# Performance work log

Measured on AMD Instinct MI355X. Metric: run time of the kernel, lower is better.

## Reference

```python
import jax, jax.numpy as jnp
import numpy as np


def setup_inputs() -> dict:
    key = jax.random.key(0)
    kp, kq, kr = jax.random.split(key, 3)
    N, M = 8192, 4096
    points = jax.random.normal(kp, (N, 3), dtype=jnp.float32)
    queries = jax.random.normal(kq, (M, 3), dtype=jnp.float32)
    radii = jax.random.uniform(kr, (M,), dtype=jnp.float32) * 0.3 + 0.1
    points_row_splits = jnp.array([0, N], dtype=jnp.int64)
    queries_row_splits = jnp.array([0, M], dtype=jnp.int64)
    return {
        "points": points,
        "queries": queries,
        "radii": radii,
        "points_row_splits": points_row_splits,
        "queries_row_splits": queries_row_splits,
    }


def reference(points, queries, radii, points_row_splits, queries_row_splits):
    """Radius search, metric=L2 (squared distances), return_distances=True.

    JIT-friendly ragged encoding: neighbors_index and neighbors_distance are
    returned as fixed-size [M*N] buffers with valid entries packed at the
    front (query-major order, matching the compact list of the original op);
    padding is -1 for indices and 0.0 for distances. neighbors_row_splits is
    the exact exclusive prefix sum of per-query neighbor counts ([M+1]).
    """
    M = queries.shape[0]
    N = points.shape[0]
    # squared L2 distances [M, N] without materializing [M, N, 3]
    q2 = jnp.sum(queries * queries, axis=1, keepdims=True)          # [M,1]
    p2 = jnp.sum(points * points, axis=1)[None, :]                  # [1,N]
    qp = jnp.einsum("md,nd->mn", queries, points)                   # [M,N]
    d2 = jnp.maximum(q2 + p2 - 2.0 * qp, 0.0)

    mask = d2 <= (radii * radii)[:, None]                           # [M,N]
    counts = jnp.sum(mask, axis=1, dtype=jnp.int64)                 # [M]
    neighbors_row_splits = jnp.concatenate(
        [jnp.zeros((1,), jnp.int64), jnp.cumsum(counts)])           # [M+1]
    total = neighbors_row_splits[-1]

    # Stable sort of the flattened (row-major) mask packs all valid slots at
    # the front while preserving query-major, point-index order.
    flat_mask = mask.reshape(-1)
    order = jnp.argsort(1 - flat_mask.astype(jnp.int32), stable=True)  # [M*N]
    valid = jnp.arange(M * N, dtype=jnp.int64) < total
    neighbors_index = jnp.where(valid, (order % N).astype(jnp.int64), -1)
    neighbors_distance = jnp.where(valid, d2.reshape(-1)[order], 0.0)
    return neighbors_index, neighbors_row_splits, neighbors_distance
```

## Files before the change

kernel.cpp:

```cpp
#include <hip/hip_runtime.h>


typedef float f32x4 __attribute__((ext_vector_type(4)));

__global__ __launch_bounds__(256) void rs_fused(
    const float* __restrict__ pts, const float* __restrict__ qs,
    const float* __restrict__ rad, int* __restrict__ counts,
    unsigned long long* __restrict__ masks, int storeMasks,
    float* __restrict__ out_idx, float* __restrict__ out_dist,
    long long MN, int N, int M) {
    int t = threadIdx.x;
    int wv = t >> 6, lane = t & 63;
    int gw = blockIdx.x * 4 + wv;
    int nWaves = gridDim.x * 4;

    bool hasQ = (gw < M);
    int qc = hasQ ? gw : 0;
    float qx = qs[3 * qc], qy = qs[3 * qc + 1], qz = qs[3 * qc + 2];
    float q2 = __fadd_rn(__fadd_rn(__fmul_rn(qx, qx), __fmul_rn(qy, qy)),
                         __fmul_rn(qz, qz));
    float r = rad[qc];
    float r2 = hasQ ? __fmul_rn(r, r) : -1.0f;

    int nc = N >> 6;
    int vecIters = N >> 8;
    long long V = MN >> 2;
    long long perWave = (V + nWaves - 1) / nWaves;
    int fillIters = (int)((perWave + 63) >> 6);
    long long fbase = (long long)gw * perWave;
    long long fend = fbase + perWave;
    if (fend > V) fend = V;
    f32x4* vidx = (f32x4*)out_idx;
    f32x4* vdst = (f32x4*)out_dist;
    f32x4 vm1 = {-1.0f, -1.0f, -1.0f, -1.0f};
    f32x4 vz = {0.0f, 0.0f, 0.0f, 0.0f};

    int iters = vecIters > fillIters ? vecIters : fillIters;
    int cntLane = 0;
    int shift = (lane & 15) << 2;
    int wordSel = lane >> 4;

    for (int it = 0; it < iters; ++it) {
        if (it < fillIters) {
            long long fi = fbase + (long long)it * 64 + lane;
            if (fi < fend) { vidx[fi] = vm1; vdst[fi] = vz; }
        }
        if (it < vecIters) {
            const f32x4* pv = (const f32x4*)(pts + (size_t)it * 768);
            f32x4 v0 = pv[3 * lane + 0];
            f32x4 v1 = pv[3 * lane + 1];
            f32x4 v2 = pv[3 * lane + 2];
            float px[4] = {v0.x, v0.w, v1.z, v2.y};
            float py[4] = {v0.y, v1.x, v1.w, v2.z};
            float pz[4] = {v0.z, v1.y, v2.x, v2.w};
            unsigned nib = 0;
#pragma unroll
            for (int k = 0; k < 4; ++k) {
                float p2 = __fadd_rn(
                    __fadd_rn(__fmul_rn(px[k], px[k]), __fmul_rn(py[k], py[k])),
                    __fmul_rn(pz[k], pz[k]));
                float qp = __fadd_rn(
                    __fadd_rn(__fmul_rn(qx, px[k]), __fmul_rn(qy, py[k])),
                    __fmul_rn(qz, pz[k]));
                float d2 = __fsub_rn(__fadd_rn(q2, p2), __fmul_rn(2.0f, qp));
                bool pred = (d2 <= r2);
                nib |= (pred ? 1u : 0u) << k;
                cntLane += pred ? 1 : 0;
            }
            unsigned long long contrib = (unsigned long long)nib << shift;
#pragma unroll
            for (int s = 1; s < 16; s <<= 1) contrib |= __shfl_xor(contrib, s, 64);
            if (storeMasks && hasQ && (lane & 15) == 0)
                masks[(long long)gw * nc + (it << 2) + wordSel] = contrib;
        }
    }
    for (int c = vecIters << 2; c < nc; ++c) {
        int p = (c << 6) + lane;
        bool vld = (p < N);
        int pcl = vld ? p : 0;
        float px = pts[3 * pcl], py = pts[3 * pcl + 1], pz = pts[3 * pcl + 2];
        float p2 = __fadd_rn(__fadd_rn(__fmul_rn(px, px), __fmul_rn(py, py)),
                             __fmul_rn(pz, pz));
        float qp = __fadd_rn(__fadd_rn(__fmul_rn(qx, px), __fmul_rn(qy, py)),
                             __fmul_rn(qz, pz));
        float d2 = __fsub_rn(__fadd_rn(q2, p2), __fmul_rn(2.0f, qp));
        bool pred = vld && (d2 <= r2);
        unsigned long long b = __ballot(pred);
        if (storeMasks && hasQ && lane == 0) masks[(long long)gw * nc + c] = b;
        cntLane += pred ? 1 : 0;
    }
    for (int off = 32; off > 0; off >>= 1) cntLane += __shfl_down(cntLane, off, 64);
    if (hasQ && lane == 0) counts[gw] = cntLane;
}

__global__ __launch_bounds__(256) void rs_write(
    const float* __restrict__ pts, const float* __restrict__ qs,
    const float* __restrict__ rad,
    const int* __restrict__ counts, const unsigned long long* __restrict__ masks,
    int useMasks,
    float* __restrict__ out_idx, float* __restrict__ out_splits,
    float* __restrict__ out_dist, int N, int M) {
    __shared__ int s_scan[256];
    __shared__ int s_split[4097];
    int t = threadIdx.x;

    {
        int c[16];
        int sum = 0;
        int b16 = t * 16;
#pragma unroll
        for (int i = 0; i < 16; ++i) {
            int idx = b16 + i;
            int v = (idx < M) ? counts[idx] : 0;
            c[i] = sum;
            sum += v;
        }
        s_scan[t] = sum;
        __syncthreads();
        for (int off = 1; off < 256; off <<= 1) {
            int add = (t >= off) ? s_scan[t - off] : 0;
            __syncthreads();
            s_scan[t] += add;
            __syncthreads();
        }
        int excl = (t == 0) ? 0 : s_scan[t - 1];
#pragma unroll
        for (int i = 0; i < 16; ++i)
            if (b16 + i < M) s_split[b16 + i] = excl + c[i];
        if (t == 255) s_split[M] = excl + sum;
        __syncthreads();
    }

    if (blockIdx.x == 0) {
        for (int i = t; i <= M; i += 256) out_splits[i] = (float)s_split[i];
    }

    int wv = t >> 6, lane = t & 63;
    int w = blockIdx.x * 4 + wv;
    if (w >= M) return;
    float qxx = qs[3 * w], qyy = qs[3 * w + 1], qzz = qs[3 * w + 2];
    float q2 = __fadd_rn(__fadd_rn(__fmul_rn(qxx, qxx), __fmul_rn(qyy, qyy)),
                         __fmul_rn(qzz, qzz));
    long long base = s_split[w];
    int nc = N >> 6;

    if (useMasks) {
        const unsigned long long* mq = masks + (long long)w * nc;
        unsigned long long w0 = (lane < nc) ? mq[lane] : 0ull;
        unsigned long long w1 = (lane + 64 < nc) ? mq[lane + 64] : 0ull;
        int c0 = __popcll(w0), c1 = __popcll(w1);
        int i0 = c0, i1 = c1;
        for (int off = 1; off < 64; off <<= 1) {
            int t0 = __shfl_up(i0, off, 64);
            int t1 = __shfl_up(i1, off, 64);
            if (lane >= off) { i0 += t0; i1 += t1; }
        }
        int total0 = __shfl(i0, 63, 64);

        long long o = base + (i0 - c0);
        int pbase = lane << 6;
        unsigned long long mm = w0;
        while (mm) {
            int b = __ffsll((long long)mm) - 1;
            int p = pbase + b;
            float px = pts[3 * p], py = pts[3 * p + 1], pz = pts[3 * p + 2];
            float p2 = __fadd_rn(__fadd_rn(__fmul_rn(px, px), __fmul_rn(py, py)),
                                 __fmul_rn(pz, pz));
            float qp = __fadd_rn(__fadd_rn(__fmul_rn(qxx, px), __fmul_rn(qyy, py)),
                                 __fmul_rn(qzz, pz));
            float d2 = fmaxf(__fsub_rn(__fadd_rn(q2, p2), __fmul_rn(2.0f, qp)), 0.0f);
            out_idx[o] = (float)p;
            out_dist[o] = d2;
            ++o;
            mm &= mm - 1;
        }
        o = base + total0 + (i1 - c1);
        pbase = (lane + 64) << 6;
        mm = w1;
        while (mm) {
            int b = __ffsll((long long)mm) - 1;
            int p = pbase + b;
            float px = pts[3 * p], py = pts[3 * p + 1], pz = pts[3 * p + 2];
            float p2 = __fadd_rn(__fadd_rn(__fmul_rn(px, px), __fmul_rn(py, py)),
                                 __fmul_rn(pz, pz));
            float qp = __fadd_rn(__fadd_rn(__fmul_rn(qxx, px), __fmul_rn(qyy, py)),
                                 __fmul_rn(qzz, pz));
            float d2 = fmaxf(__fsub_rn(__fadd_rn(q2, p2), __fmul_rn(2.0f, qp)), 0.0f);
            out_idx[o] = (float)p;
            out_dist[o] = d2;
            ++o;
            mm &= mm - 1;
        }
    } else {
        float r = rad[w];
        float r2 = __fmul_rn(r, r);
        int cum = 0;
        unsigned long long lanemask = (1ull << lane) - 1ull;
        for (int p0 = 0; p0 < N; p0 += 64) {
            int p = p0 + lane;
            float px = pts[3 * p], py = pts[3 * p + 1], pz = pts[3 * p + 2];
            float p2 = __fadd_rn(__fadd_rn(__fmul_rn(px, px), __fmul_rn(py, py)),
                                 __fmul_rn(pz, pz));
            float qp = __fadd_rn(__fadd_rn(__fmul_rn(qxx, px), __fmul_rn(qyy, py)),
                                 __fmul_rn(qzz, pz));
            float d2 = __fsub_rn(__fadd_rn(q2, p2), __fmul_rn(2.0f, qp));
            bool pred = (d2 <= r2);
            unsigned long long mask = __ballot(pred);
            if (pred) {
                long long pos = base + cum + __popcll(mask & lanemask);
                out_idx[pos] = (float)p;
                out_dist[pos] = fmaxf(d2, 0.0f);
            }
            cum += __popcll(mask);
        }
    }
}

extern "C" void kernel_launch(void* const* d_in, const int* in_sizes, int n_in,
                              void* d_out, int out_size, void* d_ws, size_t ws_size,
                              hipStream_t stream) {
    const float* points = (const float*)d_in[0];
    const float* queries = (const float*)d_in[1];
    const float* radii = (const float*)d_in[2];
    int N = in_sizes[0] / 3;
    int M = in_sizes[1] / 3;
    long long MN = (long long)M * (long long)N;

    float* out = (float*)d_out;
    float* out_idx = out;
    float* out_splits = out + MN;
    float* out_dist = out + MN + M + 1;

    char* ws = (char*)d_ws;
    size_t off = 0;
    auto take = [&](size_t bytes) -> size_t {
        size_t o = off;
        off += (bytes + 255) & ~(size_t)255;
        return o;
    };
    size_t o_counts = take((size_t)M * 4);
    size_t o_masks = take((size_t)M * (size_t)(N / 64) * 8);
    bool useMasks = (off <= ws_size) && ((N >> 6) <= 128);
    int* counts = (int*)(ws + o_counts);
    unsigned long long* masks = (unsigned long long*)(ws + o_masks);

    int C = (M + 3) / 4;
    rs_fused<<<C, 256, 0, stream>>>(points, queries, radii, counts, masks,
                                    useMasks ? 1 : 0, out_idx, out_dist, MN, N, M);
    int writeBlocks = (M + 3) / 4;
    rs_write<<<writeBlocks, 256, 0, stream>>>(points, queries, radii, counts, masks,
                                              useMasks ? 1 : 0, out_idx, out_splits,
                                              out_dist, N, M);
}
```

Before: 58.91 us.

## Skip zero-filling the distance region that later gets overwritten

The first kernel used to zero-fill the whole distance buffer before the real distances were written. That fill now happens in the second kernel, where interleaved blocks compute the total count and zero only the padding tail past it. This removes a redundant write of the valid distance prefix. It also rebalances where memory traffic lands across the two kernels, and each fill block repeats a reduction over all counts.

```diff
diff --git a/kernel.cpp b/kernel.cpp
--- a/kernel.cpp
+++ b/kernel.cpp
@@ -2,13 +2,24 @@
 
 
 typedef float f32x4 __attribute__((ext_vector_type(4)));
+
+__device__ __forceinline__ void fill_region(float* __restrict__ base, long long n,
+                                            float val, long long tid, long long nth) {
+    long long head = (long long)(((16u - ((unsigned)(size_t)base & 15u)) & 15u) >> 2);
+    if (head > n) head = n;
+    for (long long i = tid; i < head; i += nth) base[i] = val;
+    long long nv = (n - head) >> 2;
+    f32x4* v = (f32x4*)(base + head);
+    f32x4 vv = {val, val, val, val};
+    for (long long i = tid; i < nv; i += nth) v[i] = vv;
+    for (long long i = head + (nv << 2) + tid; i < n; i += nth) base[i] = val;
+}
 
 __global__ __launch_bounds__(256) void rs_fused(
     const float* __restrict__ pts, const float* __restrict__ qs,
     const float* __restrict__ rad, int* __restrict__ counts,
     unsigned long long* __restrict__ masks, int storeMasks,
-    float* __restrict__ out_idx, float* __restrict__ out_dist,
-    long long MN, int N, int M) {
+    float* __restrict__ out_idx, long long MN, int N, int M) {
     int t = threadIdx.x;
     int wv = t >> 6, lane = t & 63;
     int gw = blockIdx.x * 4 + wv;
@@ -31,9 +42,7 @@
     long long fend = fbase + perWave;
     if (fend > V) fend = V;
     f32x4* vidx = (f32x4*)out_idx;
-    f32x4* vdst = (f32x4*)out_dist;
     f32x4 vm1 = {-1.0f, -1.0f, -1.0f, -1.0f};
-    f32x4 vz = {0.0f, 0.0f, 0.0f, 0.0f};
 
     int iters = vecIters > fillIters ? vecIters : fillIters;
     int cntLane = 0;
@@ -43,7 +52,7 @@
     for (int it = 0; it < iters; ++it) {
         if (it < fillIters) {
             long long fi = fbase + (long long)it * 64 + lane;
-            if (fi < fend) { vidx[fi] = vm1; vdst[fi] = vz; }
+            if (fi < fend) vidx[fi] = vm1;
         }
         if (it < vecIters) {
             const f32x4* pv = (const f32x4*)(pts + (size_t)it * 768);
@@ -99,10 +108,37 @@
     const int* __restrict__ counts, const unsigned long long* __restrict__ masks,
     int useMasks,
     float* __restrict__ out_idx, float* __restrict__ out_splits,
-    float* __restrict__ out_dist, int N, int M) {
+    float* __restrict__ out_dist, long long MN, int N, int M, int W ) {
     __shared__ int s_scan[256];
     __shared__ int s_split[4097];
     int t = threadIdx.x;
+    int bid = blockIdx.x;
+
+    if (bid & 1) {
+        int fid = bid >> 1;
+        int sum = 0;
+        int b16 = t * 16;
+#pragma unroll
+        for (int i = 0; i < 16; ++i) {
+            int idx = b16 + i;
+            if (idx < M) sum += counts[idx];
+        }
+        s_scan[t] = sum;
+        __syncthreads();
+        for (int off = 128; off > 0; off >>= 1) {
+            if (t < off) s_scan[t] += s_scan[t + off];
+            __syncthreads();
+        }
+        long long total = s_scan[0];
+        long long padLen = MN - total;
+        if (padLen > 0) {
+            long long tid = (long long)fid * 256 + t;
+            long long nth = (long long)W * 256;
+            fill_region(out_dist + total, padLen, 0.0f, tid, nth);
+        }
+        return;
+    }
+    int wb = bid >> 1;
 
     {
         int c[16];
@@ -131,12 +167,12 @@
         __syncthreads();
     }
 
-    if (blockIdx.x == 0) {
+    if (wb == 0) {
         for (int i = t; i <= M; i += 256) out_splits[i] = (float)s_split[i];
     }
 
     int wv = t >> 6, lane = t & 63;
-    int w = blockIdx.x * 4 + wv;
+    int w = wb * 4 + wv;
     if (w >= M) return;
     float qxx = qs[3 * w], qyy = qs[3 * w + 1], qzz = qs[3 * w + 2];
     float q2 = __fadd_rn(__fadd_rn(__fmul_rn(qxx, qxx), __fmul_rn(qyy, qyy)),
@@ -246,9 +282,9 @@
 
     int C = (M + 3) / 4;
     rs_fused<<<C, 256, 0, stream>>>(points, queries, radii, counts, masks,
-                                    useMasks ? 1 : 0, out_idx, out_dist, MN, N, M);
-    int writeBlocks = (M + 3) / 4;
-    rs_write<<<writeBlocks, 256, 0, stream>>>(points, queries, radii, counts, masks,
-                                              useMasks ? 1 : 0, out_idx, out_splits,
-                                              out_dist, N, M);
-}
+                                    useMasks ? 1 : 0, out_idx, MN, N, M);
+    int W = (M + 3) / 4;
+    rs_write<<<2 * W, 256, 0, stream>>>(points, queries, radii, counts, masks,
+                                        useMasks ? 1 : 0, out_idx, out_splits,
+                                        out_dist, MN, N, M, W);
+}
```

Measured after the change: 77.02 us. 1.31x slower.

## Move prefix scan into last-finishing block of count kernel

Applied to the files above, without the earlier changes.

Before, every block of the write kernel redid the full prefix scan over all query counts in shared memory. Now the last block to finish the count kernel, found with an atomic counter and threadfence, does the scan once and writes the splits to global memory. The pack kernel then just reads its base offset. This adds a memset launch and a serialized tail scan at the end of the first kernel, and also clamps out-of-range point loads in the non-mask path.

```diff
diff --git a/kernel.cpp b/kernel.cpp
--- a/kernel.cpp
+++ b/kernel.cpp
@@ -8,7 +8,8 @@
     const float* __restrict__ rad, int* __restrict__ counts,
     unsigned long long* __restrict__ masks, int storeMasks,
     float* __restrict__ out_idx, float* __restrict__ out_dist,
-    long long MN, int N, int M) {
+    float* __restrict__ out_splits, int* __restrict__ splits_i,
+    int* __restrict__ done, long long MN, int N, int M) {
     int t = threadIdx.x;
     int wv = t >> 6, lane = t & 63;
     int gw = blockIdx.x * 4 + wv;
@@ -91,27 +92,25 @@
     }
     for (int off = 32; off > 0; off >>= 1) cntLane += __shfl_down(cntLane, off, 64);
     if (hasQ && lane == 0) counts[gw] = cntLane;
-}
-
-__global__ __launch_bounds__(256) void rs_write(
-    const float* __restrict__ pts, const float* __restrict__ qs,
-    const float* __restrict__ rad,
-    const int* __restrict__ counts, const unsigned long long* __restrict__ masks,
-    int useMasks,
-    float* __restrict__ out_idx, float* __restrict__ out_splits,
-    float* __restrict__ out_dist, int N, int M) {
+
+    __shared__ int s_last;
     __shared__ int s_scan[256];
-    __shared__ int s_split[4097];
-    int t = threadIdx.x;
-
-    {
+    __syncthreads();
+    if (t == 0) {
+        __threadfence();
+        int old = atomicAdd(done, 1);
+        s_last = (old == (int)gridDim.x - 1) ? 1 : 0;
+    }
+    __syncthreads();
+    if (s_last) {
+        volatile const int* vcounts = (volatile const int*)counts;
         int c[16];
         int sum = 0;
         int b16 = t * 16;
 #pragma unroll
         for (int i = 0; i < 16; ++i) {
             int idx = b16 + i;
-            int v = (idx < M) ? counts[idx] : 0;
+            int v = (idx < M) ? vcounts[idx] : 0;
             c[i] = sum;
             sum += v;
         }
@@ -125,23 +124,35 @@
         }
         int excl = (t == 0) ? 0 : s_scan[t - 1];
 #pragma unroll
-        for (int i = 0; i < 16; ++i)
-            if (b16 + i < M) s_split[b16 + i] = excl + c[i];
-        if (t == 255) s_split[M] = excl + sum;
-        __syncthreads();
-    }
-
-    if (blockIdx.x == 0) {
-        for (int i = t; i <= M; i += 256) out_splits[i] = (float)s_split[i];
-    }
-
+        for (int i = 0; i < 16; ++i) {
+            int idx = b16 + i;
+            if (idx < M) {
+                int v = excl + c[i];
+                splits_i[idx] = v;
+                out_splits[idx] = (float)v;
+            }
+        }
+        if (t == 255) {
+            splits_i[M] = excl + sum;
+            out_splits[M] = (float)(excl + sum);
+        }
+    }
+}
+
+__global__ __launch_bounds__(256) void rs_pack(
+    const float* __restrict__ pts, const float* __restrict__ qs,
+    const float* __restrict__ rad,
+    const int* __restrict__ splits_i, const unsigned long long* __restrict__ masks,
+    int useMasks,
+    float* __restrict__ out_idx, float* __restrict__ out_dist, int N, int M) {
+    int t = threadIdx.x;
     int wv = t >> 6, lane = t & 63;
     int w = blockIdx.x * 4 + wv;
     if (w >= M) return;
     float qxx = qs[3 * w], qyy = qs[3 * w + 1], qzz = qs[3 * w + 2];
     float q2 = __fadd_rn(__fadd_rn(__fmul_rn(qxx, qxx), __fmul_rn(qyy, qyy)),
                          __fmul_rn(qzz, qzz));
-    long long base = s_split[w];
+    long long base = splits_i[w];
     int nc = N >> 6;
 
     if (useMasks) {
@@ -198,13 +209,15 @@
         unsigned long long lanemask = (1ull << lane) - 1ull;
         for (int p0 = 0; p0 < N; p0 += 64) {
             int p = p0 + lane;
-            float px = pts[3 * p], py = pts[3 * p + 1], pz = pts[3 * p + 2];
+            bool vld = (p < N);
+            int pcl = vld ? p : 0;
+            float px = pts[3 * pcl], py = pts[3 * pcl + 1], pz = pts[3 * pcl + 2];
             float p2 = __fadd_rn(__fadd_rn(__fmul_rn(px, px), __fmul_rn(py, py)),
                                  __fmul_rn(pz, pz));
             float qp = __fadd_rn(__fadd_rn(__fmul_rn(qxx, px), __fmul_rn(qyy, py)),
                                  __fmul_rn(qzz, pz));
             float d2 = __fsub_rn(__fadd_rn(q2, p2), __fmul_rn(2.0f, qp));
-            bool pred = (d2 <= r2);
+            bool pred = vld && (d2 <= r2);
             unsigned long long mask = __ballot(pred);
             if (pred) {
                 long long pos = base + cum + __popcll(mask & lanemask);
@@ -239,16 +252,22 @@
         return o;
     };
     size_t o_counts = take((size_t)M * 4);
+    size_t o_splits = take((size_t)(M + 1) * 4);
+    size_t o_done = take(4);
     size_t o_masks = take((size_t)M * (size_t)(N / 64) * 8);
     bool useMasks = (off <= ws_size) && ((N >> 6) <= 128);
     int* counts = (int*)(ws + o_counts);
+    int* splits_i = (int*)(ws + o_splits);
+    int* done = (int*)(ws + o_done);
     unsigned long long* masks = (unsigned long long*)(ws + o_masks);
+
+    hipMemsetAsync((void*)done, 0, 4, stream);
 
     int C = (M + 3) / 4;
     rs_fused<<<C, 256, 0, stream>>>(points, queries, radii, counts, masks,
-                                    useMasks ? 1 : 0, out_idx, out_dist, MN, N, M);
-    int writeBlocks = (M + 3) / 4;
-    rs_write<<<writeBlocks, 256, 0, stream>>>(points, queries, radii, counts, masks,
-                                              useMasks ? 1 : 0, out_idx, out_splits,
-                                              out_dist, N, M);
+                                    useMasks ? 1 : 0, out_idx, out_dist, out_splits,
+                                    splits_i, done, MN, N, M);
+    int packBlocks = (M + 3) / 4;
+    rs_pack<<<packBlocks, 256, 0, stream>>>(points, queries, radii, splits_i, masks,
+                                            useMasks ? 1 : 0, out_idx, out_dist, N, M);
 }
```

After: 97.44 us. 1.65x slower.

## Split padding fill and mask compute into separate interleaved block roles

Applied to the files above, without the earlier changes.

Instead of each wave interleaving its share of the large -1/0 padding fill with its mask computation, the launch doubles the grid and assigns even blocks to compute masks and counts and odd blocks to a grid-strided vectorized fill of both output buffers, with alignment handling. This aims to let the store-bound fill and the compute-bound mask work run on different blocks concurrently and simplifies the compute loop. It also adds a bounds guard for ragged N in the write kernel's fallback path. The risk is load imbalance between the two block roles.

```diff
diff --git a/kernel.cpp b/kernel.cpp
--- a/kernel.cpp
+++ b/kernel.cpp
@@ -3,76 +3,86 @@
 
 typedef float f32x4 __attribute__((ext_vector_type(4)));
 
-__global__ __launch_bounds__(256) void rs_fused(
+__device__ __forceinline__ void fill_region(float* __restrict__ base, long long n,
+                                            float val, long long tid, long long nth) {
+    long long head = (long long)(((16u - ((unsigned)(size_t)base & 15u)) & 15u) >> 2);
+    if (head > n) head = n;
+    for (long long i = tid; i < head; i += nth) base[i] = val;
+    long long nv = (n - head) >> 2;
+    f32x4* v = (f32x4*)(base + head);
+    f32x4 vv = {val, val, val, val};
+    for (long long i = tid; i < nv; i += nth) v[i] = vv;
+    for (long long i = head + (nv << 2) + tid; i < n; i += nth) base[i] = val;
+}
+
+__global__ __launch_bounds__(256) void rs_main(
     const float* __restrict__ pts, const float* __restrict__ qs,
     const float* __restrict__ rad, int* __restrict__ counts,
     unsigned long long* __restrict__ masks, int storeMasks,
     float* __restrict__ out_idx, float* __restrict__ out_dist,
-    long long MN, int N, int M) {
+    long long MN, int N, int M, int CB, int FB) {
+    int bid = blockIdx.x;
     int t = threadIdx.x;
+
+    int cid = -1, fid = -1;
+    if (CB == FB) {
+        if ((bid & 1) == 0) cid = bid >> 1;
+        else fid = bid >> 1;
+    } else {
+        if (bid < CB) cid = bid;
+        else fid = bid - CB;
+    }
+
+    if (fid >= 0) {
+        long long tid = (long long)fid * 256 + t;
+        long long nth = (long long)FB * 256;
+        fill_region(out_idx, MN, -1.0f, tid, nth);
+        fill_region(out_dist, MN, 0.0f, tid, nth);
+        return;
+    }
+
     int wv = t >> 6, lane = t & 63;
-    int gw = blockIdx.x * 4 + wv;
-    int nWaves = gridDim.x * 4;
-
-    bool hasQ = (gw < M);
-    int qc = hasQ ? gw : 0;
-    float qx = qs[3 * qc], qy = qs[3 * qc + 1], qz = qs[3 * qc + 2];
+    int gw = cid * 4 + wv;
+    if (gw >= M) return;
+    float qx = qs[3 * gw], qy = qs[3 * gw + 1], qz = qs[3 * gw + 2];
     float q2 = __fadd_rn(__fadd_rn(__fmul_rn(qx, qx), __fmul_rn(qy, qy)),
                          __fmul_rn(qz, qz));
-    float r = rad[qc];
-    float r2 = hasQ ? __fmul_rn(r, r) : -1.0f;
+    float r = rad[gw];
+    float r2 = __fmul_rn(r, r);
 
     int nc = N >> 6;
     int vecIters = N >> 8;
-    long long V = MN >> 2;
-    long long perWave = (V + nWaves - 1) / nWaves;
-    int fillIters = (int)((perWave + 63) >> 6);
-    long long fbase = (long long)gw * perWave;
-    long long fend = fbase + perWave;
-    if (fend > V) fend = V;
-    f32x4* vidx = (f32x4*)out_idx;
-    f32x4* vdst = (f32x4*)out_dist;
-    f32x4 vm1 = {-1.0f, -1.0f, -1.0f, -1.0f};
-    f32x4 vz = {0.0f, 0.0f, 0.0f, 0.0f};
-
-    int iters = vecIters > fillIters ? vecIters : fillIters;
     int cntLane = 0;
     int shift = (lane & 15) << 2;
     int wordSel = lane >> 4;
 
-    for (int it = 0; it < iters; ++it) {
-        if (it < fillIters) {
-            long long fi = fbase + (long long)it * 64 + lane;
-            if (fi < fend) { vidx[fi] = vm1; vdst[fi] = vz; }
-        }
-        if (it < vecIters) {
-            const f32x4* pv = (const f32x4*)(pts + (size_t)it * 768);
-            f32x4 v0 = pv[3 * lane + 0];
-            f32x4 v1 = pv[3 * lane + 1];
-            f32x4 v2 = pv[3 * lane + 2];
-            float px[4] = {v0.x, v0.w, v1.z, v2.y};
-            float py[4] = {v0.y, v1.x, v1.w, v2.z};
-            float pz[4] = {v0.z, v1.y, v2.x, v2.w};
-            unsigned nib = 0;
-#pragma unroll
-            for (int k = 0; k < 4; ++k) {
-                float p2 = __fadd_rn(
-                    __fadd_rn(__fmul_rn(px[k], px[k]), __fmul_rn(py[k], py[k])),
-                    __fmul_rn(pz[k], pz[k]));
-                float qp = __fadd_rn(
-                    __fadd_rn(__fmul_rn(qx, px[k]), __fmul_rn(qy, py[k])),
-                    __fmul_rn(qz, pz[k]));
-                float d2 = __fsub_rn(__fadd_rn(q2, p2), __fmul_rn(2.0f, qp));
-                bool pred = (d2 <= r2);
-                nib |= (pred ? 1u : 0u) << k;
-                cntLane += pred ? 1 : 0;
-            }
-            unsigned long long contrib = (unsigned long long)nib << shift;
-#pragma unroll
-            for (int s = 1; s < 16; s <<= 1) contrib |= __shfl_xor(contrib, s, 64);
-            if (storeMasks && hasQ && (lane & 15) == 0)
-                masks[(long long)gw * nc + (it << 2) + wordSel] = contrib;
-        }
+    for (int it = 0; it < vecIters; ++it) {
+        const f32x4* pv = (const f32x4*)(pts + (size_t)it * 768);
+        f32x4 v0 = pv[3 * lane + 0];
+        f32x4 v1 = pv[3 * lane + 1];
+        f32x4 v2 = pv[3 * lane + 2];
+        float px[4] = {v0.x, v0.w, v1.z, v2.y};
+        float py[4] = {v0.y, v1.x, v1.w, v2.z};
+        float pz[4] = {v0.z, v1.y, v2.x, v2.w};
+        unsigned nib = 0;
+#pragma unroll
+        for (int k = 0; k < 4; ++k) {
+            float p2 = __fadd_rn(
+                __fadd_rn(__fmul_rn(px[k], px[k]), __fmul_rn(py[k], py[k])),
+                __fmul_rn(pz[k], pz[k]));
+            float qp = __fadd_rn(
+                __fadd_rn(__fmul_rn(qx, px[k]), __fmul_rn(qy, py[k])),
+                __fmul_rn(qz, pz[k]));
+            float d2 = __fsub_rn(__fadd_rn(q2, p2), __fmul_rn(2.0f, qp));
+            bool pred = (d2 <= r2);
+            nib |= (pred ? 1u : 0u) << k;
+            cntLane += pred ? 1 : 0;
+        }
+        unsigned long long contrib = (unsigned long long)nib << shift;
+#pragma unroll
+        for (int s = 1; s < 16; s <<= 1) contrib |= __shfl_xor(contrib, s, 64);
+        if (storeMasks && (lane & 15) == 0)
+            masks[(long long)gw * nc + (it << 2) + wordSel] = contrib;
     }
     for (int c = vecIters << 2; c < nc; ++c) {
         int p = (c << 6) + lane;
@@ -86,11 +96,11 @@
         float d2 = __fsub_rn(__fadd_rn(q2, p2), __fmul_rn(2.0f, qp));
         bool pred = vld && (d2 <= r2);
         unsigned long long b = __ballot(pred);
-        if (storeMasks && hasQ && lane == 0) masks[(long long)gw * nc + c] = b;
+        if (storeMasks && lane == 0) masks[(long long)gw * nc + c] = b;
         cntLane += pred ? 1 : 0;
     }
     for (int off = 32; off > 0; off >>= 1) cntLane += __shfl_down(cntLane, off, 64);
-    if (hasQ && lane == 0) counts[gw] = cntLane;
+    if (lane == 0) counts[gw] = cntLane;
 }
 
 __global__ __launch_bounds__(256) void rs_write(
@@ -198,13 +208,15 @@
         unsigned long long lanemask = (1ull << lane) - 1ull;
         for (int p0 = 0; p0 < N; p0 += 64) {
             int p = p0 + lane;
-            float px = pts[3 * p], py = pts[3 * p + 1], pz = pts[3 * p + 2];
+            bool vld = (p < N);
+            int pcl = vld ? p : 0;
+            float px = pts[3 * pcl], py = pts[3 * pcl + 1], pz = pts[3 * pcl + 2];
             float p2 = __fadd_rn(__fadd_rn(__fmul_rn(px, px), __fmul_rn(py, py)),
                                  __fmul_rn(pz, pz));
             float qp = __fadd_rn(__fadd_rn(__fmul_rn(qxx, px), __fmul_rn(qyy, py)),
                                  __fmul_rn(qzz, pz));
             float d2 = __fsub_rn(__fadd_rn(q2, p2), __fmul_rn(2.0f, qp));
-            bool pred = (d2 <= r2);
+            bool pred = vld && (d2 <= r2);
             unsigned long long mask = __ballot(pred);
             if (pred) {
                 long long pos = base + cum + __popcll(mask & lanemask);
@@ -244,9 +256,11 @@
     int* counts = (int*)(ws + o_counts);
     unsigned long long* masks = (unsigned long long*)(ws + o_masks);
 
-    int C = (M + 3) / 4;
-    rs_fused<<<C, 256, 0, stream>>>(points, queries, radii, counts, masks,
-                                    useMasks ? 1 : 0, out_idx, out_dist, MN, N, M);
+    int CB = (M + 3) / 4;
+    int FB = CB;
+    rs_main<<<CB + FB, 256, 0, stream>>>(points, queries, radii, counts, masks,
+                                         useMasks ? 1 : 0, out_idx, out_dist, MN, N, M,
+                                         CB, FB);
     int writeBlocks = (M + 3) / 4;
     rs_write<<<writeBlocks, 256, 0, stream>>>(points, queries, radii, counts, masks,
                                               useMasks ? 1 : 0, out_idx, out_splits,
```

Result: slower. 76.70 us (+30.2%).
